# Kernel optimization log

Hardware: AMD Instinct MI355X
Metric: run time of the kernel (lower is better)

## Reference

```python
import jax, jax.numpy as jnp
import numpy as np

N_GOOD = 16
NUM_TEST = 16
NUM_UNITS = 32
EPS = 1e-5


def _mlp(x, w1, b1, w2, b2):
    # Linear -> ReLU -> Linear -> ReLU
    h = jax.nn.relu(x @ w1 + b1)
    return jax.nn.relu(h @ w2 + b2)


def _ln_relu(x, g, b):
    mu = jnp.mean(x, axis=-1, keepdims=True)
    var = jnp.mean(jnp.square(x - mu), axis=-1, keepdims=True)
    return jax.nn.relu((x - mu) / jnp.sqrt(var + EPS) * g + b)


def _attend(self_out, enc):
    # self_out: [B, D], enc: [B, N, D]
    scores = jnp.einsum('bd,bnd->bn', self_out, enc) / np.float32(np.sqrt(NUM_TEST))
    attn = jax.nn.softmax(scores, axis=-1)
    return jnp.einsum('bn,bnd->bd', attn, enc)


def setup_inputs() -> dict:
    key = jax.random.key(0)
    ks = jax.random.split(key, 24)
    B = 262144
    obs_dim = 4 + (N_GOOD - 1) * 5 + N_GOOD * 3  # 127

    def lin(k, fan_in, fan_out):
        bound = 1.0 / np.sqrt(fan_in)
        kw, kb = jax.random.split(k)
        w = jax.random.uniform(kw, (fan_in, fan_out), jnp.float32, -bound, bound)
        b = jax.random.uniform(kb, (fan_out,), jnp.float32, -bound, bound)
        return w, b

    en_w1, en_b1 = lin(ks[0], 4, NUM_UNITS)
    en_w2, en_b2 = lin(ks[1], NUM_UNITS, NUM_TEST)
    oa_w1, oa_b1 = lin(ks[2], 5, NUM_UNITS)
    oa_w2, oa_b2 = lin(ks[3], NUM_UNITS, NUM_TEST)
    g_w1, g_b1 = lin(ks[4], 3, NUM_UNITS)
    g_w2, g_b2 = lin(ks[5], NUM_UNITS, NUM_TEST)
    m_w1, m_b1 = lin(ks[6], NUM_TEST * 3, NUM_UNITS)
    m_w2, m_b2 = lin(ks[7], NUM_UNITS, NUM_UNITS)
    m_w3, m_b3 = lin(ks[8], NUM_UNITS, 2)

    return {
        's_input': jax.random.normal(ks[9], (B, obs_dim), jnp.float32),
        'en_w1': en_w1, 'en_b1': en_b1, 'en_w2': en_w2, 'en_b2': en_b2,
        'oa_w1': oa_w1, 'oa_b1': oa_b1, 'oa_w2': oa_w2, 'oa_b2': oa_b2,
        'oa_g': jnp.ones((NUM_TEST,), jnp.float32), 'oa_bln': jnp.zeros((NUM_TEST,), jnp.float32),
        'g_w1': g_w1, 'g_b1': g_b1, 'g_w2': g_w2, 'g_b2': g_b2,
        'g_g': jnp.ones((NUM_TEST,), jnp.float32), 'g_bln': jnp.zeros((NUM_TEST,), jnp.float32),
        'm_w1': m_w1, 'm_b1': m_b1, 'm_w2': m_w2, 'm_b2': m_b2, 'm_w3': m_w3, 'm_b3': m_b3,
    }


def reference(s_input, en_w1, en_b1, en_w2, en_b2,
              oa_w1, oa_b1, oa_w2, oa_b2, oa_g, oa_bln,
              g_w1, g_b1, g_w2, g_b2, g_g, g_bln,
              m_w1, m_b1, m_w2, m_b2, m_w3, m_b3):
    n = N_GOOD
    B = s_input.shape[0]

    # self encoding: [B, 16]
    self_out = _mlp(s_input[:, :4], en_w1, en_b1, en_w2, en_b2)

    # other agents: width (n-1)*5 = [pos pairs | vel pairs | scalar per agent]
    og = s_input[:, 4:4 + (n - 1) * 5]
    pos = og[:, :(n - 1) * 2].reshape(B, n - 1, 2)
    vel = og[:, (n - 1) * 2:(n - 1) * 4].reshape(B, n - 1, 2)
    scal = og[:, (n - 1) * 4:(n - 1) * 5].reshape(B, n - 1, 1)
    other_in = jnp.concatenate([pos, vel, scal], axis=-1)  # [B, n-1, 5]
    other_enc = _mlp(other_in, oa_w1, oa_b1, oa_w2, oa_b2)  # [B, n-1, 16]
    other_out = _ln_relu(_attend(self_out, other_enc), oa_g, oa_bln)

    # food/goals: last n*3 cols, chunks of 3
    food_in = s_input[:, -n * 3:].reshape(B, n, 3)
    food_enc = _mlp(food_in, g_w1, g_b1, g_w2, g_b2)  # [B, n, 16]
    food_out = _ln_relu(_attend(self_out, food_enc), g_g, g_bln)

    merged = jnp.concatenate([self_out, food_out, other_out], axis=1)  # [B, 48]
    h = jax.nn.leaky_relu(merged @ m_w1 + m_b1, 0.01)
    h = jax.nn.leaky_relu(h @ m_w2 + m_b2, 0.01)
    return jnp.tanh(h @ m_w3 + m_b3)  # [B, 2]
```

## Files before the change

### kernel.cpp

```cpp
#include <hip/hip_runtime.h>


#define OBS 127
#define RSTR 200
#define ZROW (32 * RSTR)
#define WWORDS (33 * RSTR)

typedef _Float16 v8h  __attribute__((ext_vector_type(8)));
typedef _Float16 v8ha __attribute__((ext_vector_type(8), aligned(16)));
typedef float    f32x8 __attribute__((ext_vector_type(8)));
typedef float    v16f __attribute__((ext_vector_type(16)));
typedef float    f4u  __attribute__((ext_vector_type(4), aligned(4)));
typedef float    f2u  __attribute__((ext_vector_type(2), aligned(4)));
typedef unsigned ui2  __attribute__((ext_vector_type(2), aligned(8)));
typedef unsigned ui4  __attribute__((ext_vector_type(4), aligned(16)));

#define MFMA16(a, b, c) __builtin_amdgcn_mfma_f32_32x32x16_f16((a), (b), (c), 0, 0, 0)

__device__ __forceinline__ unsigned pkw(float a, float b) {
    return __builtin_bit_cast(unsigned, __builtin_amdgcn_cvt_pkrtz(a, b));
}
__device__ __forceinline__ v8h zero8h() {
    v8h z;
    #pragma unroll
    for (int j = 0; j < 8; ++j) z[j] = (_Float16)0.f;
    return z;
}
__device__ __forceinline__ v8h pk8(const v16f& d, int b) {
    ui4 u;
    u[0] = pkw(d[b],     d[b + 1]);
    u[1] = pkw(d[b + 2], d[b + 3]);
    u[2] = pkw(d[b + 4], d[b + 5]);
    u[3] = pkw(d[b + 6], d[b + 7]);
    return __builtin_bit_cast(v8h, u);
}
__device__ __forceinline__ v8h pkr8(const v16f& d, int b) {
    return __builtin_elementwise_max(pk8(d, b), zero8h());
}
__device__ __forceinline__ v8h pk8v(f32x8 v) {
    ui4 u;
    u[0] = pkw(v[0], v[1]);
    u[1] = pkw(v[2], v[3]);
    u[2] = pkw(v[4], v[5]);
    u[3] = pkw(v[6], v[7]);
    return __builtin_bit_cast(v8h, u);
}
__device__ __forceinline__ v8h lrelu8(v8h t) {
    const v8h s = t * (_Float16)0.01f;
    return __builtin_elementwise_max(t, s);
}
__device__ __forceinline__ v8h a1fragK16(const float* __restrict__ W,
                                         const float* __restrict__ b,
                                         int kin, int m, int h) {
    const int Lm = (m & ~12) | ((m & 4) << 1) | ((m & 8) >> 1);
    v8h r;
    #pragma unroll
    for (int j = 0; j < 8; ++j) {
        const int k = 8 * h + j;
        const float v = (k < kin) ? W[k * 32 + Lm] : (k == kin ? b[Lm] : 0.f);
        r[j] = (_Float16)v;
    }
    return r;
}
__device__ __forceinline__ v8h a2fragK16(const float* __restrict__ W2,
                                         int s, int m, int h) {
    v8h r;
    #pragma unroll
    for (int j = 0; j < 8; ++j)
        r[j] = (_Float16)((m < 16) ? W2[(16 * s + 8 * h + j) * 16 + m] : 0.f);
    return r;
}
__device__ __forceinline__ v8h mfragK16(const float* __restrict__ W, int ncols,
                                        int base, int m, int h, int colmax) {
    v8h r;
    #pragma unroll
    for (int j = 0; j < 8; ++j) {
        const int ch = base + (j & 3) + 8 * (j >> 2) + 4 * h;
        r[j] = (_Float16)((m < colmax) ? W[ch * ncols + m] : 0.f);
    }
    return r;
}
__device__ __forceinline__ float fast_tanh(float x) {
    x = fminf(fmaxf(x, -15.f), 15.f);
    const float ex = __expf(2.f * x);
    return (ex - 1.f) / (ex + 1.f);
}

__device__ __forceinline__ v8h ld16h(const _Float16* p) {
    return *(const v8ha*)p;
}
__device__ __forceinline__ v8h ld8h(const _Float16* p) {
    const ui2 w = *(const ui2*)p;
    ui4 u;
    u[0] = w[0]; u[1] = w[1]; u[2] = 0u; u[3] = 0u;
    return __builtin_bit_cast(v8h, u);
}

__device__ __forceinline__ void estep(v8h bf, v8h A1, v8h A2a, v8h A2b,
                                      f32x8 b2v, f32x8 stl,
                                      float& l, f32x8& o, v16f z16) {
    const v16f dH = MFMA16(A1, bf, z16);
    const v8h p0 = pkr8(dH, 0);
    const v8h p1 = pkr8(dH, 8);
    v16f c = MFMA16(A2a, p0, z16);
    c = MFMA16(A2b, p1, c);
    f32x8 e2;
    #pragma unroll
    for (int r = 0; r < 8; ++r) e2[r] = fmaxf(c[r] + b2v[r], 0.f);
    float part = 0.f;
    #pragma unroll
    for (int r = 0; r < 8; ++r) part += stl[r] * e2[r];
    part += __shfl_xor(part, 32);
    const float p = __builtin_amdgcn_exp2f(part);
    l += p;
    o += p * e2;
}

__device__ __forceinline__ v8h ln_fin(float l, f32x8 o, f32x8 gv, f32x8 blv) {
    const float rl = 1.f / l;
    f32x8 a = o * rl;
    float sum = 0.f;
    #pragma unroll
    for (int r = 0; r < 8; ++r) sum += a[r];
    sum += __shfl_xor(sum, 32);
    const float mu = sum * 0.0625f;
    a -= mu;
    float var = 0.f;
    #pragma unroll
    for (int r = 0; r < 8; ++r) var += a[r] * a[r];
    var += __shfl_xor(var, 32);
    const float inv = rsqrtf(var * 0.0625f + 1e-5f);
    f32x8 v;
    #pragma unroll
    for (int r = 0; r < 8; ++r) v[r] = fmaxf(a[r] * inv * gv[r] + blv[r], 0.f);
    return pk8v(v);
}

__global__ __launch_bounds__(256)
void actor_mfma(const float* __restrict__ x,
                const float* __restrict__ en_w1, const float* __restrict__ en_b1,
                const float* __restrict__ en_w2, const float* __restrict__ en_b2,
                const float* __restrict__ oa_w1, const float* __restrict__ oa_b1,
                const float* __restrict__ oa_w2, const float* __restrict__ oa_b2,
                const float* __restrict__ oa_g,  const float* __restrict__ oa_bln,
                const float* __restrict__ g_w1,  const float* __restrict__ g_b1,
                const float* __restrict__ g_w2,  const float* __restrict__ g_b2,
                const float* __restrict__ g_g,   const float* __restrict__ g_bln,
                const float* __restrict__ m_w1,  const float* __restrict__ m_b1,
                const float* __restrict__ m_w2,  const float* __restrict__ m_b2,
                const float* __restrict__ m_w3,  const float* __restrict__ m_b3,
                float* __restrict__ out, int B)
{
    const int lane = threadIdx.x & 63, wid = threadIdx.x >> 6;
    const int n = lane & 31, h = lane >> 5;

    __shared__ __align__(16) _Float16 xs_all[4][WWORDS];
    _Float16* xs = xs_all[wid];

    const int r0 = blockIdx.x * 128 + wid * 32;
    int rows = B - r0;
    rows = rows > 32 ? 32 : (rows < 0 ? 0 : rows);

    if (lane < 24) {
        ui4 z;
        z[0] = 0u; z[1] = 0u; z[2] = 0u; z[3] = 0u;
        *(ui4*)(xs + ZROW + lane * 8) = z;
    }

    if (rows > 0) {
        const float* __restrict__ xp = x + (size_t)r0 * OBS;
        if (lane < rows) {
            const f4u v = *(const f4u*)(xp + lane * OBS);
            ui4 q;
            q[0] = pkw(v[0], v[1]);
            q[1] = pkw(v[2], v[3]);
            q[2] = pkw(1.f, 0.f);
            q[3] = 0u;
            *(ui4*)(xs + lane * RSTR) = q;
        }
        #pragma unroll
        for (int i = 0; i < 8; ++i) {
            const int t = i * 64 + lane, row = t >> 4, e = t & 15;
            if (row < rows) {
                const f4u v = *(const f4u*)(xp + row * OBS + 78 + 3 * e);
                ui2 w;
                w[0] = pkw(v[1], v[2]);
                w[1] = pkw(v[3], 1.f);
                *(ui2*)(xs + row * RSTR + 8 + 4 * e) = w;
            }
        }
        #pragma unroll
        for (int i = 0; i < 8; ++i) {
            const int t = i * 64 + lane, row = t >> 4, e = t & 15;
            if (e < 15 && row < rows) {
                const float* rp = xp + row * OBS;
                const f2u pv = *(const f2u*)(rp + 4 + 2 * e);
                const f2u vv = *(const f2u*)(rp + 34 + 2 * e);
                const float sc = rp[64 + e];
                ui4 q;
                q[0] = pkw(pv[0], pv[1]);
                q[1] = pkw(vv[0], vv[1]);
                q[2] = pkw(sc, 1.f);
                q[3] = 0u;
                *(ui4*)(xs + row * RSTR + 72 + 8 * e) = q;
            }
        }
    }

    v16f z16;
    #pragma unroll
    for (int r = 0; r < 16; ++r) z16[r] = 0.f;

    f32x8 sb2v, fb2v, ob2v;
    #pragma unroll
    for (int r = 0; r < 8; ++r) {
        const int m = (r & 3) + 8 * (r >> 2) + 4 * h;
        sb2v[r] = en_b2[m];
        fb2v[r] = g_b2[m];
        ob2v[r] = oa_b2[m];
    }

    const int rbase = h ? ZROW : n * RSTR;

    f32x8 stl;
    v8h Bs;
    {
        const v8h sA1 = a1fragK16(en_w1, en_b1, 4, n, h);
        const v8h sA2a = a2fragK16(en_w2, 0, n, h);
        const v8h sA2b = a2fragK16(en_w2, 1, n, h);
        const v8h bs = ld16h(xs + rbase);
        const v16f dS = MFMA16(sA1, bs, z16);
        v16f cS = MFMA16(sA2a, pkr8(dS, 0), z16);
        cS = MFMA16(sA2b, pkr8(dS, 8), cS);
        const float SK = 0.25f * 1.44269504088896f;
        f32x8 sv;
        #pragma unroll
        for (int r = 0; r < 8; ++r) sv[r] = fmaxf(cS[r] + sb2v[r], 0.f);
        stl = sv * SK;
        Bs = pk8v(sv);
    }

    const v8h fA1 = a1fragK16(g_w1, g_b1, 3, n, h);
    const v8h fA2a = a2fragK16(g_w2, 0, n, h);
    const v8h fA2b = a2fragK16(g_w2, 1, n, h);
    const v8h oA1 = a1fragK16(oa_w1, oa_b1, 5, n, h);
    const v8h oA2a = a2fragK16(oa_w2, 0, n, h);
    const v8h oA2b = a2fragK16(oa_w2, 1, n, h);

    float lf = 0.f, lo = 0.f;
    f32x8 of = 0.f, oo = 0.f;
    #pragma unroll 2
    for (int e = 0; e < 16; ++e) {
        const v8h bfF = ld8h(xs + rbase + 8 + 4 * e);
        estep(bfF, fA1, fA2a, fA2b, fb2v, stl, lf, of, z16);
        if (e < 15) {
            const v8h bfO = ld16h(xs + rbase + 72 + 8 * e);
            estep(bfO, oA1, oA2a, oA2b, ob2v, stl, lo, oo, z16);
        }
    }

    f32x8 fgv, fblv, ogv, oblv;
    #pragma unroll
    for (int r = 0; r < 8; ++r) {
        const int m = (r & 3) + 8 * (r >> 2) + 4 * h;
        fgv[r] = g_g[m];  fblv[r] = g_bln[m];
        ogv[r] = oa_g[m]; oblv[r] = oa_bln[m];
    }
    const v8h Bf = ln_fin(lf, of, fgv, fblv);
    const v8h Bo = ln_fin(lo, oo, ogv, oblv);

    v16f m1C, m2C;
    #pragma unroll
    for (int r = 0; r < 16; ++r) {
        const int m = (r & 3) + 8 * (r >> 2) + 4 * h;
        m1C[r] = m_b1[m];
        m2C[r] = m_b2[m];
    }
    v16f m1 = MFMA16(mfragK16(m_w1, 32, 0, n, h, 32), Bs, m1C);
    m1 = MFMA16(mfragK16(m_w1, 32, 16, n, h, 32), Bf, m1);
    m1 = MFMA16(mfragK16(m_w1, 32, 32, n, h, 32), Bo, m1);
    const v8h q0 = lrelu8(pk8(m1, 0));
    const v8h q1 = lrelu8(pk8(m1, 8));
    v16f m2 = MFMA16(mfragK16(m_w2, 32, 0, n, h, 32), q0, m2C);
    m2 = MFMA16(mfragK16(m_w2, 32, 16, n, h, 32), q1, m2);
    const v8h z0 = lrelu8(pk8(m2, 0));
    const v8h z1 = lrelu8(pk8(m2, 8));
    v16f m3 = MFMA16(mfragK16(m_w3, 2, 0, n, h, 2), z0, z16);
    m3 = MFMA16(mfragK16(m_w3, 2, 16, n, h, 2), z1, m3);

    if (h == 0 && n < rows) {
        float2 res;
        res.x = fast_tanh(m3[0] + m_b3[0]);
        res.y = fast_tanh(m3[1] + m_b3[1]);
        *(float2*)(out + (size_t)(r0 + n) * 2) = res;
    }
}

extern "C" void kernel_launch(void* const* d_in, const int* in_sizes, int n_in,
                              void* d_out, int out_size, void* d_ws, size_t ws_size,
                              hipStream_t stream) {
    const int B = in_sizes[0] / OBS;
    const float* xin = (const float*)d_in[0];
    const float* en_w1 = (const float*)d_in[1];
    const float* en_b1 = (const float*)d_in[2];
    const float* en_w2 = (const float*)d_in[3];
    const float* en_b2 = (const float*)d_in[4];
    const float* oa_w1 = (const float*)d_in[5];
    const float* oa_b1 = (const float*)d_in[6];
    const float* oa_w2 = (const float*)d_in[7];
    const float* oa_b2 = (const float*)d_in[8];
    const float* oa_g  = (const float*)d_in[9];
    const float* oa_bl = (const float*)d_in[10];
    const float* g_w1  = (const float*)d_in[11];
    const float* g_b1  = (const float*)d_in[12];
    const float* g_w2  = (const float*)d_in[13];
    const float* g_b2  = (const float*)d_in[14];
    const float* g_g   = (const float*)d_in[15];
    const float* g_bl  = (const float*)d_in[16];
    const float* m_w1  = (const float*)d_in[17];
    const float* m_b1  = (const float*)d_in[18];
    const float* m_w2  = (const float*)d_in[19];
    const float* m_b2  = (const float*)d_in[20];
    const float* m_w3  = (const float*)d_in[21];
    const float* m_b3  = (const float*)d_in[22];

    const int rows_per_block = 128;
    const int grid = (B + rows_per_block - 1) / rows_per_block;
    actor_mfma<<<grid, 256, 0, stream>>>(
        xin, en_w1, en_b1, en_w2, en_b2,
        oa_w1, oa_b1, oa_w2, oa_b2, oa_g, oa_bl,
        g_w1, g_b1, g_w2, g_b2, g_g, g_bl,
        m_w1, m_b1, m_w2, m_b2, m_w3, m_b3,
        (float*)d_out, B);
}
```

Before: 313.0 us.

## Batch attention entity steps to overlap MFMA chains and shuffles

```diff
diff --git a/kernel.cpp b/kernel.cpp
--- a/kernel.cpp
+++ b/kernel.cpp
@@ -95,25 +95,43 @@
     u[0] = w[0]; u[1] = w[1]; u[2] = 0u; u[3] = 0u;
     return __builtin_bit_cast(v8h, u);
 }
-
-__device__ __forceinline__ void estep(v8h bf, v8h A1, v8h A2a, v8h A2b,
-                                      f32x8 b2v, f32x8 stl,
-                                      float& l, f32x8& o, v16f z16) {
-    const v16f dH = MFMA16(A1, bf, z16);
-    const v8h p0 = pkr8(dH, 0);
-    const v8h p1 = pkr8(dH, 8);
-    v16f c = MFMA16(A2a, p0, z16);
-    c = MFMA16(A2b, p1, c);
-    f32x8 e2;
-    #pragma unroll
-    for (int r = 0; r < 8; ++r) e2[r] = fmaxf(c[r] + b2v[r], 0.f);
-    float part = 0.f;
-    #pragma unroll
-    for (int r = 0; r < 8; ++r) part += stl[r] * e2[r];
-    part += __shfl_xor(part, 32);
-    const float p = __builtin_amdgcn_exp2f(part);
-    l += p;
-    o += p * e2;
+__device__ __forceinline__ float dot8(f32x8 a, f32x8 b) {
+    float s0 = a[0] * b[0], s1 = a[1] * b[1];
+    float s2 = a[2] * b[2], s3 = a[3] * b[3];
+    s0 += a[4] * b[4]; s1 += a[5] * b[5];
+    s2 += a[6] * b[6]; s3 += a[7] * b[7];
+    return (s0 + s1) + (s2 + s3);
+}
+
+template <int CNT, bool FOOD>
+__device__ __forceinline__ void ebatch(const _Float16* xr, int e0,
+                                       v8h A1, v8h A2a, v8h A2b,
+                                       f32x8 b2v, f32x8 stl,
+                                       float& l, f32x8& o, v16f z16) {
+    f32x8 e2s[CNT];
+    float dt[CNT];
+    #pragma unroll
+    for (int i = 0; i < CNT; ++i) {
+        const int e = e0 + i;
+        const v8h bf = FOOD ? ld8h(xr + 8 + 4 * e) : ld16h(xr + 72 + 8 * e);
+        const v16f dH = MFMA16(A1, bf, z16);
+        v16f c = MFMA16(A2a, pkr8(dH, 0), z16);
+        c = MFMA16(A2b, pkr8(dH, 8), c);
+        f32x8 e2;
+        #pragma unroll
+        for (int r = 0; r < 8; ++r) e2[r] = fmaxf(c[r] + b2v[r], 0.f);
+        e2s[i] = e2;
+        dt[i] = dot8(stl, e2);
+    }
+    float sc[CNT];
+    #pragma unroll
+    for (int i = 0; i < CNT; ++i) sc[i] = dt[i] + __shfl_xor(dt[i], 32);
+    #pragma unroll
+    for (int i = 0; i < CNT; ++i) {
+        const float p = __builtin_amdgcn_exp2f(sc[i]);
+        l += p;
+        o += p * e2s[i];
+    }
 }
 
 __device__ __forceinline__ v8h ln_fin(float l, f32x8 o, f32x8 gv, f32x8 blv) {
@@ -136,7 +154,7 @@
     return pk8v(v);
 }
 
-__global__ __launch_bounds__(256)
+__global__ __launch_bounds__(256, 3)
 void actor_mfma(const float* __restrict__ x,
                 const float* __restrict__ en_w1, const float* __restrict__ en_b1,
                 const float* __restrict__ en_w2, const float* __restrict__ en_b2,
@@ -221,6 +239,7 @@
     }
 
     const int rbase = h ? ZROW : n * RSTR;
+    const _Float16* xr = xs + rbase;
 
     f32x8 stl;
     v8h Bs;
@@ -228,7 +247,7 @@
         const v8h sA1 = a1fragK16(en_w1, en_b1, 4, n, h);
         const v8h sA2a = a2fragK16(en_w2, 0, n, h);
         const v8h sA2b = a2fragK16(en_w2, 1, n, h);
-        const v8h bs = ld16h(xs + rbase);
+        const v8h bs = ld16h(xr);
         const v16f dS = MFMA16(sA1, bs, z16);
         v16f cS = MFMA16(sA2a, pkr8(dS, 0), z16);
         cS = MFMA16(sA2b, pkr8(dS, 8), cS);
@@ -240,23 +259,24 @@
         Bs = pk8v(sv);
     }
 
-    const v8h fA1 = a1fragK16(g_w1, g_b1, 3, n, h);
-    const v8h fA2a = a2fragK16(g_w2, 0, n, h);
-    const v8h fA2b = a2fragK16(g_w2, 1, n, h);
-    const v8h oA1 = a1fragK16(oa_w1, oa_b1, 5, n, h);
-    const v8h oA2a = a2fragK16(oa_w2, 0, n, h);
-    const v8h oA2b = a2fragK16(oa_w2, 1, n, h);
-
-    float lf = 0.f, lo = 0.f;
-    f32x8 of = 0.f, oo = 0.f;
-    #pragma unroll 2
-    for (int e = 0; e < 16; ++e) {
-        const v8h bfF = ld8h(xs + rbase + 8 + 4 * e);
-        estep(bfF, fA1, fA2a, fA2b, fb2v, stl, lf, of, z16);
-        if (e < 15) {
-            const v8h bfO = ld16h(xs + rbase + 72 + 8 * e);
-            estep(bfO, oA1, oA2a, oA2b, ob2v, stl, lo, oo, z16);
-        }
+    float lf = 0.f;
+    f32x8 of = 0.f;
+    {
+        const v8h fA1 = a1fragK16(g_w1, g_b1, 3, n, h);
+        const v8h fA2a = a2fragK16(g_w2, 0, n, h);
+        const v8h fA2b = a2fragK16(g_w2, 1, n, h);
+        ebatch<8, true>(xr, 0, fA1, fA2a, fA2b, fb2v, stl, lf, of, z16);
+        ebatch<8, true>(xr, 8, fA1, fA2a, fA2b, fb2v, stl, lf, of, z16);
+    }
+
+    float lo = 0.f;
+    f32x8 oo = 0.f;
+    {
+        const v8h oA1 = a1fragK16(oa_w1, oa_b1, 5, n, h);
+        const v8h oA2a = a2fragK16(oa_w2, 0, n, h);
+        const v8h oA2b = a2fragK16(oa_w2, 1, n, h);
+        ebatch<8, false>(xr, 0, oA1, oA2a, oA2b, ob2v, stl, lo, oo, z16);
+        ebatch<7, false>(xr, 8, oA1, oA2a, oA2b, ob2v, stl, lo, oo, z16);
     }
 
     f32x8 fgv, fblv, ogv, oblv;
```

New measurement: 393.1 us. 25.6% more time.
